# Optimization experiments

Measured on AMD Instinct MI355X. Metric: run time of the kernel, lower is better.

## Reference

```python
import jax, jax.numpy as jnp
import numpy as np

N_NODES = 50000
N_EDGES = 800000
F_DIM = 35   # num_features = in_channels = out_channels
K_HOPS = 3   # num_filters (diffusion order)


def _dconv(xcat, src, dst, w_fwd, w_bwd, theta, bias, n):
    """Dual-direction diffusion convolution: sum_k T_fwd^k X theta[0,k] + T_bwd^k X theta[1,k] + b.
    xcat: [n, Cin]; theta: [2, K, Cin, Cout]; w_fwd/w_bwd: [E] normalized edge weights."""
    out = xcat @ (theta[0, 0] + theta[1, 0]) + bias  # k=0 term (identity hop)
    xf = xcat
    xb = xcat
    for k in range(1, theta.shape[1]):
        # forward diffusion: aggregate src -> dst with out-degree normalization
        xf = jax.ops.segment_sum(w_fwd[:, None] * xf[src], dst, num_segments=n)
        # backward diffusion: aggregate dst -> src with in-degree normalization
        xb = jax.ops.segment_sum(w_bwd[:, None] * xb[dst], src, num_segments=n)
        out = out + xf @ theta[0, k] + xb @ theta[1, k]
    return out


def _cell(x, h, src, dst, wf, wb, tz, bz, tr, br, tc, bc, n):
    """DCRNN GRU cell with diffusion convolutions as the gate transforms."""
    xh = jnp.concatenate([x, h], axis=-1)  # [n, 2F]
    z = jax.nn.sigmoid(_dconv(xh, src, dst, wf, wb, tz, bz, n))
    r = jax.nn.sigmoid(_dconv(xh, src, dst, wf, wb, tr, br, n))
    c = jnp.tanh(_dconv(jnp.concatenate([x, r * h], axis=-1), src, dst, wf, wb, tc, bc, n))
    return z * h + (1.0 - z) * c


def setup_inputs() -> dict:
    key = jax.random.key(0)
    ks = jax.random.split(key, 12)
    x = jax.random.normal(ks[0], (N_NODES, F_DIM), dtype=jnp.float32)
    edge_index = jax.random.randint(ks[1], (2, N_EDGES), 0, N_NODES)
    edge_weight = jax.random.uniform(ks[2], (N_EDGES,), dtype=jnp.float32)
    cin = 2 * F_DIM
    s = 1.0 / np.sqrt(cin)
    u = lambda k, sh: jax.random.uniform(k, sh, jnp.float32, -s, s)
    theta_z = u(ks[3], (2, K_HOPS, cin, F_DIM)); b_z = u(ks[4], (F_DIM,))
    theta_r = u(ks[5], (2, K_HOPS, cin, F_DIM)); b_r = u(ks[6], (F_DIM,))
    theta_c = u(ks[7], (2, K_HOPS, cin, F_DIM)); b_c = u(ks[8], (F_DIM,))
    sl = 1.0 / np.sqrt(F_DIM)
    W_lin = jax.random.uniform(ks[9], (F_DIM, 1), jnp.float32, -sl, sl)
    b_lin = jax.random.uniform(ks[10], (1,), jnp.float32, -sl, sl)
    return dict(x=x, edge_index=edge_index, edge_weight=edge_weight,
                theta_z=theta_z, b_z=b_z, theta_r=theta_r, b_r=b_r,
                theta_c=theta_c, b_c=b_c, W_lin=W_lin, b_lin=b_lin)


def reference(x, edge_index, edge_weight, theta_z, b_z, theta_r, b_r, theta_c, b_c, W_lin, b_lin):
    n = x.shape[0]
    src, dst = edge_index[0], edge_index[1]
    # learned/normalized adjacency A (forward + backward transition weights)
    deg_out = jax.ops.segment_sum(edge_weight, src, num_segments=n)
    deg_in = jax.ops.segment_sum(edge_weight, dst, num_segments=n)
    wf = edge_weight / jnp.where(deg_out[src] > 0, deg_out[src], 1.0)
    wb = edge_weight / jnp.where(deg_in[dst] > 0, deg_in[dst], 1.0)
    A = jnp.stack([wf, wb])  # [2, E]
    h = jnp.zeros_like(x)
    # recurrent cell called twice (second call reuses hidden state and A)
    h = _cell(x, h, src, dst, wf, wb, theta_z, b_z, theta_r, b_r, theta_c, b_c, n)
    h = _cell(x, h, src, dst, wf, wb, theta_z, b_z, theta_r, b_r, theta_c, b_c, n)
    out = jax.nn.relu(h @ W_lin + b_lin)  # [n, 1]
    return out, A
```

## Files before the change

### kernel.cpp

```cpp
#include <hip/hip_runtime.h>
#include <hip/hip_fp16.h>

#define NF 35
#define HS 36
#define TMAT 2450
#define ZCOLS 384
#define ZUSED 360
#define CCOLS 192
#define CUSED 180


__global__ void degree2_k(const int* __restrict__ src, const int* __restrict__ dst,
                          unsigned int* __restrict__ cntF2, unsigned int* __restrict__ cntB2,
                          int* __restrict__ rankF, int* __restrict__ rankB, int E) {
    int e = blockIdx.x * blockDim.x + threadIdx.x;
    if (e < E) {
        int d = dst[e], s = src[e];
        int shd = (d & 1) * 16, shs = (s & 1) * 16;
        unsigned int o1 = atomicAdd(&cntF2[d >> 1], 1u << shd);
        rankF[e] = (int)((o1 >> shd) & 0xFFFFu);
        unsigned int o2 = atomicAdd(&cntB2[s >> 1], 1u << shs);
        rankB[e] = (int)((o2 >> shs) & 0xFFFFu);
    }
}

__global__ __launch_bounds__(1024) void scan2_k(const unsigned int* __restrict__ cntF2,
                                                const unsigned int* __restrict__ cntB2,
                                                int* __restrict__ rowF,
                                                int* __restrict__ rowB, int n) {
    const unsigned int* cnt = blockIdx.x ? cntB2 : cntF2;
    int* row = blockIdx.x ? rowB : rowF;
    __shared__ int wsum[16];
    __shared__ int carry_s;
    int lane = threadIdx.x & 63, wid = threadIdx.x >> 6;
    if (threadIdx.x == 0) carry_s = 0;
    __syncthreads();
    for (int base = 0; base < n; base += 1024) {
        int i = base + threadIdx.x;
        int v = 0;
        if (i < n) v = (int)((cnt[i >> 1] >> ((i & 1) * 16)) & 0xFFFFu);
        int s = v;
        for (int off = 1; off < 64; off <<= 1) {
            int t = __shfl_up(s, off, 64);
            if (lane >= off) s += t;
        }
        if (lane == 63) wsum[wid] = s;
        __syncthreads();
        if (wid == 0) {
            int t = (lane < 16) ? wsum[lane] : 0;
            int ss = t;
            for (int off = 1; off < 16; off <<= 1) {
                int u = __shfl_up(ss, off, 64);
                if (lane >= off) ss += u;
            }
            if (lane < 16) wsum[lane] = ss - t;
        }
        __syncthreads();
        if (i < n) row[i] = carry_s + wsum[wid] + s - v;
        __syncthreads();
        if (threadIdx.x == 1023) carry_s += wsum[15] + s;
        __syncthreads();
    }
    if (threadIdx.x == 0) row[n] = carry_s;
}

__global__ void scatter2_k(const int* __restrict__ src, const int* __restrict__ dst,
                           const float* __restrict__ w,
                           const int* __restrict__ rankF, const int* __restrict__ rankB,
                           const int* __restrict__ rowF, const int* __restrict__ rowB,
                           int2* __restrict__ pairF, int2* __restrict__ pairB, int E) {
    int e = blockIdx.x * blockDim.x + threadIdx.x;
    if (e < E) {
        int s = src[e], d = dst[e];
        int wb = __float_as_int(w[e]);
        pairF[rowF[d] + rankF[e]] = make_int2(s, wb);
        pairB[rowB[s] + rankB[e]] = make_int2(d, wb);
    }
}

__global__ void segdeg_k(const int* __restrict__ rowF, const int* __restrict__ rowB,
                         const int2* __restrict__ pairF, const int2* __restrict__ pairB,
                         float* __restrict__ deg_in, float* __restrict__ deg_out, int n) {
    int i = blockIdx.x * blockDim.x + threadIdx.x;
    if (i >= n) return;
    float a = 0.f;
    for (int p = rowF[i]; p < rowF[i + 1]; ++p) a += __int_as_float(pairF[p].y);
    deg_in[i] = a;
    float b = 0.f;
    for (int p = rowB[i]; p < rowB[i + 1]; ++p) b += __int_as_float(pairB[p].y);
    deg_out[i] = b;
}

__global__ void norm_k(const int* __restrict__ src, const int* __restrict__ dst,
                       const float* __restrict__ w, const float* __restrict__ deg_out,
                       const float* __restrict__ deg_in,
                       const int2* __restrict__ pairF, const int2* __restrict__ pairB,
                       unsigned int* __restrict__ pFp, unsigned int* __restrict__ pBp,
                       float* __restrict__ wf, float* __restrict__ wb, int E) {
    int e = blockIdx.x * blockDim.x + threadIdx.x;
    if (e >= E) return;
    float ww = w[e];
    float a = deg_out[src[e]];
    float b = deg_in[dst[e]];
    wf[e] = ww / (a > 0.f ? a : 1.f);
    wb[e] = ww / (b > 0.f ? b : 1.f);
    int2 pa = pairF[e];
    float da = deg_out[pa.x];
    float wa = __int_as_float(pa.y) / (da > 0.f ? da : 1.f);
    pFp[e] = (unsigned int)pa.x |
             ((unsigned int)__half_as_ushort(__float2half_rn(wa)) << 16);
    int2 pb = pairB[e];
    float db = deg_in[pb.x];
    float wbv = __int_as_float(pb.y) / (db > 0.f ? db : 1.f);
    pBp[e] = (unsigned int)pb.x |
             ((unsigned int)__half_as_ushort(__float2half_rn(wbv)) << 16);
}


__global__ void pack_k(const float* __restrict__ tz, const float* __restrict__ tr_,
                       const float* __restrict__ tc, const float* __restrict__ bz,
                       const float* __restrict__ br, const float* __restrict__ bc,
                       float* __restrict__ PZ, float* __restrict__ PC) {
    int i = blockIdx.x * 256 + threadIdx.x;
    const int tot1 = 71 * ZCOLS;
    if (i < tot1) {
        int r = i / ZCOLS, j = i - r * ZCOLS;
        int s = j / 36, jl = j - s * 36;
        float v = 0.f;
        if (s < 10 && jl < 35) {
            int zr = s & 1;
            const float* th = zr ? tr_ : tz;
            int grp = s >> 1;
            if (r < 70) {
                if (grp == 0) v = th[r * 35 + jl] + th[3 * TMAT + r * 35 + jl];
                else {
                    int off = (grp == 1) ? 1 : (grp == 2) ? 2 : (grp == 3) ? 4 : 5;
                    v = th[off * TMAT + r * 35 + jl];
                }
            } else if (grp == 0) {
                v = zr ? br[jl] : bz[jl];
            }
        }
        PZ[i] = v;
    } else {
        int i2 = i - tot1;
        if (i2 < 71 * CCOLS) {
            int r = i2 / CCOLS, j = i2 - r * CCOLS;
            int s = j / 36, jl = j - s * 36;
            float v = 0.f;
            if (s < 5 && jl < 35) {
                if (r < 70) {
                    if (s == 0) v = tc[r * 35 + jl] + tc[3 * TMAT + r * 35 + jl];
                    else {
                        int off = (s == 1) ? 1 : (s == 2) ? 2 : (s == 3) ? 4 : 5;
                        v = tc[off * TMAT + r * 35 + jl];
                    }
                } else if (s == 0) v = bc[jl];
            }
            PC[i2] = v;
        }
    }
}


__device__ __forceinline__ uint2 pack4h(float4 a) {
    __half2 lo = __floats2half2_rn(a.x, a.y);
    __half2 hi = __floats2half2_rn(a.z, a.w);
    uint2 r;
    r.x = *(unsigned int*)&lo;
    r.y = *(unsigned int*)&hi;
    return r;
}

__device__ __forceinline__ void fma4h(float* acc, uint2 v, float w) {
    const __half2* hp = (const __half2*)&v;
#pragma unroll
    for (int k = 0; k < 2; ++k) {
        float2 f = __half22float2(hp[k]);
        acc[2 * k] += w * f.x;
        acc[2 * k + 1] += w * f.y;
    }
}

__device__ __forceinline__ void ld12h(float* a, const char* p) {
    uint2 v0 = *(const uint2*)p, v1 = *(const uint2*)(p + 8), v2 = *(const uint2*)(p + 16);
    for (int k = 0; k < 12; ++k) a[k] = 0.f;
    fma4h(a, v0, 1.f); fma4h(a + 4, v1, 1.f); fma4h(a + 8, v2, 1.f);
}

__device__ __forceinline__ void st12h(const float* a, char* p) {
    *(uint2*)p = pack4h(make_float4(a[0], a[1], a[2], a[3]));
    *(uint2*)(p + 8) = pack4h(make_float4(a[4], a[5], a[6], a[7]));
    *(uint2*)(p + 16) = pack4h(make_float4(a[8], a[9], a[10], a[11]));
}

__device__ __forceinline__ float hw(unsigned int e) {
    return __half2float(__ushort_as_half((unsigned short)(e >> 16)));
}

__device__ __forceinline__ void gath(float* acc, const char* slab, int off,
                                     const int* __restrict__ rp,
                                     const unsigned int* __restrict__ pp, int row) {
    int p = rp[row], p1 = rp[row + 1];
    for (; p + 3 < p1; p += 4) {
        unsigned int e0 = pp[p], e1 = pp[p + 1], e2 = pp[p + 2], e3 = pp[p + 3];
        const char* s0 = slab + (size_t)(e0 & 0xFFFFu) * 72 + off;
        const char* s1 = slab + (size_t)(e1 & 0xFFFFu) * 72 + off;
        const char* s2 = slab + (size_t)(e2 & 0xFFFFu) * 72 + off;
        const char* s3 = slab + (size_t)(e3 & 0xFFFFu) * 72 + off;
        uint2 a0 = *(const uint2*)s0, a1 = *(const uint2*)(s0 + 8), a2 = *(const uint2*)(s0 + 16);
        uint2 b0 = *(const uint2*)s1, b1 = *(const uint2*)(s1 + 8), b2 = *(const uint2*)(s1 + 16);
        uint2 c0 = *(const uint2*)s2, c1 = *(const uint2*)(s2 + 8), c2 = *(const uint2*)(s2 + 16);
        uint2 d0 = *(const uint2*)s3, d1 = *(const uint2*)(s3 + 8), d2 = *(const uint2*)(s3 + 16);
        float w0 = hw(e0), w1 = hw(e1), w2 = hw(e2), w3 = hw(e3);
        fma4h(acc, a0, w0); fma4h(acc + 4, a1, w0); fma4h(acc + 8, a2, w0);
        fma4h(acc, b0, w1); fma4h(acc + 4, b1, w1); fma4h(acc + 8, b2, w1);
        fma4h(acc, c0, w2); fma4h(acc + 4, c1, w2); fma4h(acc + 8, c2, w2);
        fma4h(acc, d0, w3); fma4h(acc + 4, d1, w3); fma4h(acc + 8, d2, w3);
    }
    for (; p < p1; ++p) {
        unsigned int e0 = pp[p];
        const char* s0 = slab + (size_t)(e0 & 0xFFFFu) * 72 + off;
        float w0 = hw(e0);
        fma4h(acc, *(const uint2*)s0, w0);
        fma4h(acc + 4, *(const uint2*)(s0 + 8), w0);
        fma4h(acc + 8, *(const uint2*)(s0 + 16), w0);
    }
}


template <int WCOLS, int USED>
__device__ __forceinline__ void gemm_store(const float* sxr, const float* __restrict__ W,
                                           char* OUT, size_t slb, int grow, bool valid,
                                           int wid) {
#pragma unroll
    for (int jt = 0; jt < WCOLS / 64; ++jt) {
        int j0 = __builtin_amdgcn_readfirstlane(jt * 64 + wid * 16);
        if (j0 >= USED) continue;
        const float4* bw = (const float4*)(W + (size_t)70 * WCOLS + j0);
        float4 a0 = bw[0], a1 = bw[1], a2 = bw[2], a3 = bw[3];
        for (int c = 0; c < 70; ++c) {
            float v = sxr[c];
            const float4* wr = (const float4*)(W + (size_t)c * WCOLS + j0);
            float4 w0 = wr[0], w1 = wr[1], w2 = wr[2], w3 = wr[3];
            a0.x += v * w0.x; a0.y += v * w0.y; a0.z += v * w0.z; a0.w += v * w0.w;
            a1.x += v * w1.x; a1.y += v * w1.y; a1.z += v * w1.z; a1.w += v * w1.w;
            a2.x += v * w2.x; a2.y += v * w2.y; a2.z += v * w2.z; a2.w += v * w2.w;
            a3.x += v * w3.x; a3.y += v * w3.y; a3.z += v * w3.z; a3.w += v * w3.w;
        }
        if (valid) {
            float4 as[4] = {a0, a1, a2, a3};
#pragma unroll
            for (int g = 0; g < 4; ++g) {
                int jc = j0 + 4 * g;
                if (jc >= USED) break;
                int s = jc / 36, off = jc - s * 36;
                *(uint2*)(OUT + (size_t)s * slb + (size_t)grow * 72 + off * 2) =
                    pack4h(as[g]);
            }
        }
    }
}


__global__ __launch_bounds__(256) void mm_z_k(const float* __restrict__ x,
                                              const float* __restrict__ h,
                                              const float* __restrict__ W,
                                              char* __restrict__ zS, int n) {
    __shared__ float sx[64 * 73];
    int row0 = blockIdx.x * 64;
    for (int t = threadIdx.x; t < 64 * 35; t += 256) {
        int rl = t / 35, c = t - rl * 35;
        int grow = row0 + rl;
        sx[rl * 73 + c] = (grow < n) ? x[(size_t)grow * 35 + c] : 0.f;
    }
    for (int t = threadIdx.x; t < 64 * 35; t += 256) {
        int rl = t / 35, c = t - rl * 35;
        int grow = row0 + rl;
        sx[rl * 73 + 35 + c] = (grow < n) ? h[(size_t)grow * HS + c] : 0.f;
    }
    __syncthreads();
    int lane = threadIdx.x & 63;
    int wid = threadIdx.x >> 6;
    int grow = row0 + lane;
    gemm_store<ZCOLS, ZUSED>(&sx[lane * 73], W, zS, (size_t)n * 72, grow, grow < n, wid);
}


__global__ __launch_bounds__(256) void hopAz_k(char* __restrict__ zS,
                                               const int* __restrict__ rowF,
                                               const int* __restrict__ rowB,
                                               const unsigned int* __restrict__ pF,
                                               const unsigned int* __restrict__ pB,
                                               int n) {
    size_t slb = (size_t)n * 72;
    int i = blockIdx.x * 256 + threadIdx.x;
    int row = i / 3, t = i - row * 3;
    int off = 24 * t;
    bool act = (i < n * 3);
    float acc[12];
#define HOPA_PHASE(DSTS, SRCS, RP, PP)                           \
    if (act) {                                                   \
        char* wp = zS + (DSTS)*slb + (size_t)row * 72 + off;     \
        ld12h(acc, wp);                                          \
        gath(acc, zS + (SRCS)*slb, off, RP, PP, row);            \
        st12h(acc, wp);                                          \
    }                                                            \
    __syncthreads();
    HOPA_PHASE(2, 4, rowF, pF)
    HOPA_PHASE(3, 5, rowF, pF)
    HOPA_PHASE(6, 8, rowB, pB)
    HOPA_PHASE(7, 9, rowB, pB)
#undef HOPA_PHASE
}


__global__ __launch_bounds__(256) void hopBz_k(char* __restrict__ zS,
                                               const int* __restrict__ rowF,
                                               const int* __restrict__ rowB,
                                               const unsigned int* __restrict__ pF,
                                               const unsigned int* __restrict__ pB,
                                               int n) {
    size_t slb = (size_t)n * 72;
    int i = blockIdx.x * 256 + threadIdx.x;
    int row = i / 3, t = i - row * 3;
    int off = 24 * t;
    bool act = (i < n * 3);
    float acc[12];
    if (act) {
        ld12h(acc, zS + (size_t)row * 72 + off);
        gath(acc, zS + 2 * slb, off, rowF, pF, row);
    }
    __syncthreads();
    if (act) {
        gath(acc, zS + 6 * slb, off, rowB, pB, row);
#pragma unroll
        for (int k = 0; k < 12; ++k) acc[k] = 1.f / (1.f + expf(-acc[k]));
        st12h(acc, zS + (size_t)row * 72 + off);
    }
    __syncthreads();
    if (act) {
        ld12h(acc, zS + slb + (size_t)row * 72 + off);
        gath(acc, zS + 3 * slb, off, rowF, pF, row);
    }
    __syncthreads();
    if (act) {
        gath(acc, zS + 7 * slb, off, rowB, pB, row);
#pragma unroll
        for (int k = 0; k < 12; ++k) acc[k] = 1.f / (1.f + expf(-acc[k]));
        st12h(acc, zS + slb + (size_t)row * 72 + off);
    }
}


__global__ __launch_bounds__(256) void mmc_k(const float* __restrict__ x,
                                             const float* __restrict__ h,
                                             const char* __restrict__ zS,
                                             const float* __restrict__ W,
                                             char* __restrict__ cS, int n) {
    __shared__ float sx[64 * 73];
    size_t slb = (size_t)n * 72;
    int row0 = blockIdx.x * 64;
    for (int t = threadIdx.x; t < 64 * 35; t += 256) {
        int rl = t / 35, c = t - rl * 35;
        int grow = row0 + rl;
        sx[rl * 73 + c] = (grow < n) ? x[(size_t)grow * 35 + c] : 0.f;
    }
    for (int t = threadIdx.x; t < 64 * 35; t += 256) {
        int rl = t / 35, c = t - rl * 35;
        int grow = row0 + rl;
        float v = 0.f;
        if (grow < n) {
            float r = __half2float(*(const __half*)(zS + slb + (size_t)grow * 72 + 2 * c));
            v = r * h[(size_t)grow * HS + c];
        }
        sx[rl * 73 + 35 + c] = v;
    }
    __syncthreads();
    int lane = threadIdx.x & 63;
    int wid = threadIdx.x >> 6;
    int grow = row0 + lane;
    gemm_store<CCOLS, CUSED>(&sx[lane * 73], W, cS, slb, grow, grow < n, wid);
}


__global__ __launch_bounds__(256) void hopAc_k(char* __restrict__ cS,
                                               const int* __restrict__ rowF,
                                               const int* __restrict__ rowB,
                                               const unsigned int* __restrict__ pF,
                                               const unsigned int* __restrict__ pB,
                                               int n) {
    size_t slb = (size_t)n * 72;
    int i = blockIdx.x * 256 + threadIdx.x;
    int row = i / 3, t = i - row * 3;
    int off = 24 * t;
    bool act = (i < n * 3);
    float acc[12];
    if (act) {
        char* wp = cS + slb + (size_t)row * 72 + off;
        ld12h(acc, wp);
        gath(acc, cS + 2 * slb, off, rowF, pF, row);
        st12h(acc, wp);
    }
    __syncthreads();
    if (act) {
        char* wp = cS + 3 * slb + (size_t)row * 72 + off;
        ld12h(acc, wp);
        gath(acc, cS + 4 * slb, off, rowB, pB, row);
        st12h(acc, wp);
    }
}


template <int FIN>
__global__ __launch_bounds__(256) void fch_k(const float* __restrict__ x,
                                             float* __restrict__ h,
                                             const char* __restrict__ cS,
                                             const char* __restrict__ zS,
                                             const float* __restrict__ W,
                                             char* __restrict__ zOut,
                                             const int* __restrict__ rowF,
                                             const int* __restrict__ rowB,
                                             const unsigned int* __restrict__ pF,
                                             const unsigned int* __restrict__ pB,
                                             const float* __restrict__ Wl,
                                             const float* __restrict__ bl,
                                             float* __restrict__ out, int n) {
    __shared__ float sx[64 * 73];
    __shared__ float sred[64 * 3];
    size_t slb = (size_t)n * 72;
    int row0 = blockIdx.x * 64;
    int u = threadIdx.x;
    int rl = u / 3, t = u - rl * 3;
    int row = row0 + rl;
    int off = 24 * t;
    bool act = (u < 192 && row < n);
    float acc[12];
    if (act) {
        ld12h(acc, cS + (size_t)row * 72 + off);
        gath(acc, cS + slb, off, rowF, pF, row);
    }
    __syncthreads();
    if (act) {
        gath(acc, cS + 3 * slb, off, rowB, pB, row);
        float zv[12];
        ld12h(zv, zS + (size_t)row * 72 + off);
        float* hp = h + (size_t)row * HS + 12 * t;
        float4 h0 = *(float4*)hp, h1 = *(float4*)(hp + 4), h2 = *(float4*)(hp + 8);
        float hv[12] = {h0.x, h0.y, h0.z, h0.w, h1.x, h1.y, h1.z, h1.w,
                        h2.x, h2.y, h2.z, h2.w};
#pragma unroll
        for (int k = 0; k < 12; ++k) {
            float c = tanhf(acc[k]);
            hv[k] = zv[k] * hv[k] + (1.f - zv[k]) * c;
        }
        if (FIN == 0) {
            *(float4*)hp = make_float4(hv[0], hv[1], hv[2], hv[3]);
            *(float4*)(hp + 4) = make_float4(hv[4], hv[5], hv[6], hv[7]);
            *(float4*)(hp + 8) = make_float4(hv[8], hv[9], hv[10], hv[11]);
#pragma unroll
            for (int k = 0; k < 12; ++k) sx[rl * 73 + 35 + 12 * t + k] = hv[k];
        } else {
            float part = 0.f;
#pragma unroll
            for (int k = 0; k < 12; ++k) {
                int col = 12 * t + k;
                if (col < 35) part += hv[k] * Wl[col];
            }
            sred[rl * 3 + t] = part;
        }
    }
    __syncthreads();
    if (FIN == 1) {
        if (u < 64) {
            int r2 = row0 + u;
            if (r2 < n) {
                float s = bl[0] + sred[u * 3] + sred[u * 3 + 1] + sred[u * 3 + 2];
                out[r2] = fmaxf(s, 0.f);
            }
        }
        return;
    }
    for (int t2 = threadIdx.x; t2 < 64 * 35; t2 += 256) {
        int rl2 = t2 / 35, c = t2 - rl2 * 35;
        int grow = row0 + rl2;
        sx[rl2 * 73 + c] = (grow < n) ? x[(size_t)grow * 35 + c] : 0.f;
    }
    __syncthreads();
    int lane = threadIdx.x & 63;
    int wid = threadIdx.x >> 6;
    int grow = row0 + lane;
    gemm_store<ZCOLS, ZUSED>(&sx[lane * 73], W, zOut, slb, grow, grow < n, wid);
}


extern "C" void kernel_launch(void* const* d_in, const int* in_sizes, int n_in,
                              void* d_out, int out_size, void* d_ws, size_t ws_size,
                              hipStream_t stream) {
    const float* x   = (const float*)d_in[0];
    const int*   ei  = (const int*)d_in[1];
    const float* w   = (const float*)d_in[2];
    const float* tz  = (const float*)d_in[3];
    const float* bz  = (const float*)d_in[4];
    const float* tr_ = (const float*)d_in[5];
    const float* br  = (const float*)d_in[6];
    const float* tc  = (const float*)d_in[7];
    const float* bc  = (const float*)d_in[8];
    const float* Wl  = (const float*)d_in[9];
    const float* bl  = (const float*)d_in[10];

    const int n = in_sizes[0] / NF;
    const int E = in_sizes[2];
    const int* src = ei;
    const int* dst = ei + E;

    float* out = (float*)d_out;
    float* wf = out + n;
    float* wb = wf + E;

    char* p = (char*)d_ws;
    auto alloc = [&](size_t bytes) {
        char* r = p;
        p += (bytes + 15) & ~(size_t)15;
        return r;
    };
    int2* pairF = (int2*)alloc((size_t)E * 8);
    int2* pairB = (int2*)alloc((size_t)E * 8);
    unsigned int* pFp = (unsigned int*)alloc((size_t)E * 4);
    unsigned int* pBp = (unsigned int*)alloc((size_t)E * 4);
    int* rowF = (int*)alloc((size_t)(n + 1) * 4);
    int* rowB = (int*)alloc((size_t)(n + 1) * 4);
    unsigned int* cntF2 = (unsigned int*)alloc((size_t)((n + 1) / 2 + 4) * 4);
    unsigned int* cntB2 = (unsigned int*)alloc((size_t)((n + 1) / 2 + 4) * 4);
    float* deg_in  = (float*)alloc((size_t)n * 4);
    float* deg_out = (float*)alloc((size_t)n * 4);
    float* h  = (float*)alloc((size_t)n * HS * 4);
    char* zS  = alloc((size_t)n * 72 * 10);
    char* cS  = alloc((size_t)n * 72 * 5);
    float* PZ = (float*)alloc((size_t)71 * ZCOLS * 4);
    float* PC = (float*)alloc((size_t)71 * CCOLS * 4);
    int* rankF = (int*)zS;
    int* rankB = rankF + E;

    const int gridE = (E + 255) / 256;
    const int gridN = (n + 255) / 256;
    const int g64 = (n + 63) / 64;
    const int g3 = (n * 3 + 255) / 256;
    const size_t cntBytes = ((size_t)((n + 1) / 2 + 4) * 4 + 15) & ~(size_t)15;

    hipMemsetAsync(cntF2, 0, 2 * cntBytes, stream);
    hipMemsetAsync(h, 0, (size_t)n * HS * sizeof(float), stream);
    degree2_k<<<gridE, 256, 0, stream>>>(src, dst, cntF2, cntB2, rankF, rankB, E);
    scan2_k<<<2, 1024, 0, stream>>>(cntF2, cntB2, rowF, rowB, n);
    scatter2_k<<<gridE, 256, 0, stream>>>(src, dst, w, rankF, rankB, rowF, rowB,
                                          pairF, pairB, E);
    segdeg_k<<<gridN, 256, 0, stream>>>(rowF, rowB, pairF, pairB, deg_in, deg_out, n);
    norm_k<<<gridE, 256, 0, stream>>>(src, dst, w, deg_out, deg_in, pairF, pairB,
                                      pFp, pBp, wf, wb, E);
    pack_k<<<(71 * (ZCOLS + CCOLS) + 255) / 256, 256, 0, stream>>>(tz, tr_, tc,
                                                                   bz, br, bc, PZ, PC);

    mm_z_k<<<g64, 256, 0, stream>>>(x, h, PZ, zS, n);
    hopAz_k<<<g3, 256, 0, stream>>>(zS, rowF, rowB, pFp, pBp, n);
    hopBz_k<<<g3, 256, 0, stream>>>(zS, rowF, rowB, pFp, pBp, n);
    mmc_k<<<g64, 256, 0, stream>>>(x, h, zS, PC, cS, n);
    hopAc_k<<<g3, 256, 0, stream>>>(cS, rowF, rowB, pFp, pBp, n);
    fch_k<0><<<g64, 256, 0, stream>>>(x, h, cS, zS, PZ, zS, rowF, rowB, pFp, pBp,
                                      Wl, bl, out, n);
    hopAz_k<<<g3, 256, 0, stream>>>(zS, rowF, rowB, pFp, pBp, n);
    hopBz_k<<<g3, 256, 0, stream>>>(zS, rowF, rowB, pFp, pBp, n);
    mmc_k<<<g64, 256, 0, stream>>>(x, h, zS, PC, cS, n);
    hopAc_k<<<g3, 256, 0, stream>>>(cS, rowF, rowB, pFp, pBp, n);
    fch_k<1><<<g64, 256, 0, stream>>>(x, h, cS, zS, PZ, zS, rowF, rowB, pFp, pBp,
                                      Wl, bl, out, n);
}
```

Measured before the change: 752.9 us.

## Split hop gathers into 8-byte-per-thread passes, unfuse gate kernel, skip zero hidden

The hop kernels now give each thread an 8-byte chunk (9 threads per row instead of 3) and spread independent diffusion passes across blockIdx.y instead of running them serially with __syncthreads, which raises parallelism and memory-level concurrency in the gather. The fused final-gate plus next-z GEMM kernel is replaced by a separate gate/update kernel, a templated z GEMM that skips the h half when h is zero, and a small output kernel. In exchange there are more index loads per row, smaller gathers per thread, and extra launches and round trips through global memory.

```diff
diff --git a/kernel.cpp b/kernel.cpp
--- a/kernel.cpp
+++ b/kernel.cpp
@@ -172,59 +172,50 @@
     return r;
 }
 
-__device__ __forceinline__ void fma4h(float* acc, uint2 v, float w) {
-    const __half2* hp = (const __half2*)&v;
-#pragma unroll
-    for (int k = 0; k < 2; ++k) {
-        float2 f = __half22float2(hp[k]);
-        acc[2 * k] += w * f.x;
-        acc[2 * k + 1] += w * f.y;
-    }
-}
-
-__device__ __forceinline__ void ld12h(float* a, const char* p) {
-    uint2 v0 = *(const uint2*)p, v1 = *(const uint2*)(p + 8), v2 = *(const uint2*)(p + 16);
-    for (int k = 0; k < 12; ++k) a[k] = 0.f;
-    fma4h(a, v0, 1.f); fma4h(a + 4, v1, 1.f); fma4h(a + 8, v2, 1.f);
-}
-
-__device__ __forceinline__ void st12h(const float* a, char* p) {
+__device__ __forceinline__ void fma2h(float* a, unsigned int v, float w) {
+    float2 f = __half22float2(*(__half2*)&v);
+    a[0] += w * f.x;
+    a[1] += w * f.y;
+}
+
+__device__ __forceinline__ void fma4u2(float* a, uint2 v, float w) {
+    fma2h(a, v.x, w);
+    fma2h(a + 2, v.y, w);
+}
+
+__device__ __forceinline__ void ld4h(float* a, const char* p) {
+    uint2 v = *(const uint2*)p;
+    a[0] = 0.f; a[1] = 0.f; a[2] = 0.f; a[3] = 0.f;
+    fma4u2(a, v, 1.f);
+}
+
+__device__ __forceinline__ void st4h(const float* a, char* p) {
     *(uint2*)p = pack4h(make_float4(a[0], a[1], a[2], a[3]));
-    *(uint2*)(p + 8) = pack4h(make_float4(a[4], a[5], a[6], a[7]));
-    *(uint2*)(p + 16) = pack4h(make_float4(a[8], a[9], a[10], a[11]));
 }
 
 __device__ __forceinline__ float hw(unsigned int e) {
     return __half2float(__ushort_as_half((unsigned short)(e >> 16)));
 }
 
-__device__ __forceinline__ void gath(float* acc, const char* slab, int off,
-                                     const int* __restrict__ rp,
-                                     const unsigned int* __restrict__ pp, int row) {
+__device__ __forceinline__ void gath8(float* acc, const char* slab, int off,
+                                      const int* __restrict__ rp,
+                                      const unsigned int* __restrict__ pp, int row) {
     int p = rp[row], p1 = rp[row + 1];
     for (; p + 3 < p1; p += 4) {
         unsigned int e0 = pp[p], e1 = pp[p + 1], e2 = pp[p + 2], e3 = pp[p + 3];
-        const char* s0 = slab + (size_t)(e0 & 0xFFFFu) * 72 + off;
-        const char* s1 = slab + (size_t)(e1 & 0xFFFFu) * 72 + off;
-        const char* s2 = slab + (size_t)(e2 & 0xFFFFu) * 72 + off;
-        const char* s3 = slab + (size_t)(e3 & 0xFFFFu) * 72 + off;
-        uint2 a0 = *(const uint2*)s0, a1 = *(const uint2*)(s0 + 8), a2 = *(const uint2*)(s0 + 16);
-        uint2 b0 = *(const uint2*)s1, b1 = *(const uint2*)(s1 + 8), b2 = *(const uint2*)(s1 + 16);
-        uint2 c0 = *(const uint2*)s2, c1 = *(const uint2*)(s2 + 8), c2 = *(const uint2*)(s2 + 16);
-        uint2 d0 = *(const uint2*)s3, d1 = *(const uint2*)(s3 + 8), d2 = *(const uint2*)(s3 + 16);
-        float w0 = hw(e0), w1 = hw(e1), w2 = hw(e2), w3 = hw(e3);
-        fma4h(acc, a0, w0); fma4h(acc + 4, a1, w0); fma4h(acc + 8, a2, w0);
-        fma4h(acc, b0, w1); fma4h(acc + 4, b1, w1); fma4h(acc + 8, b2, w1);
-        fma4h(acc, c0, w2); fma4h(acc + 4, c1, w2); fma4h(acc + 8, c2, w2);
-        fma4h(acc, d0, w3); fma4h(acc + 4, d1, w3); fma4h(acc + 8, d2, w3);
+        uint2 v0 = *(const uint2*)(slab + (size_t)(e0 & 0xFFFFu) * 72 + off);
+        uint2 v1 = *(const uint2*)(slab + (size_t)(e1 & 0xFFFFu) * 72 + off);
+        uint2 v2 = *(const uint2*)(slab + (size_t)(e2 & 0xFFFFu) * 72 + off);
+        uint2 v3 = *(const uint2*)(slab + (size_t)(e3 & 0xFFFFu) * 72 + off);
+        fma4u2(acc, v0, hw(e0));
+        fma4u2(acc, v1, hw(e1));
+        fma4u2(acc, v2, hw(e2));
+        fma4u2(acc, v3, hw(e3));
     }
     for (; p < p1; ++p) {
         unsigned int e0 = pp[p];
-        const char* s0 = slab + (size_t)(e0 & 0xFFFFu) * 72 + off;
-        float w0 = hw(e0);
-        fma4h(acc, *(const uint2*)s0, w0);
-        fma4h(acc + 4, *(const uint2*)(s0 + 8), w0);
-        fma4h(acc + 8, *(const uint2*)(s0 + 16), w0);
+        uint2 v0 = *(const uint2*)(slab + (size_t)(e0 & 0xFFFFu) * 72 + off);
+        fma4u2(acc, v0, hw(e0));
     }
 }
 
@@ -232,14 +223,14 @@
 template <int WCOLS, int USED>
 __device__ __forceinline__ void gemm_store(const float* sxr, const float* __restrict__ W,
                                            char* OUT, size_t slb, int grow, bool valid,
-                                           int wid) {
+                                           int wid, int kdim) {
 #pragma unroll
     for (int jt = 0; jt < WCOLS / 64; ++jt) {
         int j0 = __builtin_amdgcn_readfirstlane(jt * 64 + wid * 16);
         if (j0 >= USED) continue;
         const float4* bw = (const float4*)(W + (size_t)70 * WCOLS + j0);
         float4 a0 = bw[0], a1 = bw[1], a2 = bw[2], a3 = bw[3];
-        for (int c = 0; c < 70; ++c) {
+        for (int c = 0; c < kdim; ++c) {
             float v = sxr[c];
             const float4* wr = (const float4*)(W + (size_t)c * WCOLS + j0);
             float4 w0 = wr[0], w1 = wr[1], w2 = wr[2], w3 = wr[3];
@@ -263,6 +254,7 @@
 }
 
 
+template <int H0>
 __global__ __launch_bounds__(256) void mm_z_k(const float* __restrict__ x,
                                               const float* __restrict__ h,
                                               const float* __restrict__ W,
@@ -274,82 +266,19 @@
         int grow = row0 + rl;
         sx[rl * 73 + c] = (grow < n) ? x[(size_t)grow * 35 + c] : 0.f;
     }
-    for (int t = threadIdx.x; t < 64 * 35; t += 256) {
-        int rl = t / 35, c = t - rl * 35;
-        int grow = row0 + rl;
-        sx[rl * 73 + 35 + c] = (grow < n) ? h[(size_t)grow * HS + c] : 0.f;
+    if (!H0) {
+        for (int t = threadIdx.x; t < 64 * 35; t += 256) {
+            int rl = t / 35, c = t - rl * 35;
+            int grow = row0 + rl;
+            sx[rl * 73 + 35 + c] = (grow < n) ? h[(size_t)grow * HS + c] : 0.f;
+        }
     }
     __syncthreads();
     int lane = threadIdx.x & 63;
     int wid = threadIdx.x >> 6;
     int grow = row0 + lane;
-    gemm_store<ZCOLS, ZUSED>(&sx[lane * 73], W, zS, (size_t)n * 72, grow, grow < n, wid);
-}
-
-
-__global__ __launch_bounds__(256) void hopAz_k(char* __restrict__ zS,
-                                               const int* __restrict__ rowF,
-                                               const int* __restrict__ rowB,
-                                               const unsigned int* __restrict__ pF,
-                                               const unsigned int* __restrict__ pB,
-                                               int n) {
-    size_t slb = (size_t)n * 72;
-    int i = blockIdx.x * 256 + threadIdx.x;
-    int row = i / 3, t = i - row * 3;
-    int off = 24 * t;
-    bool act = (i < n * 3);
-    float acc[12];
-#define HOPA_PHASE(DSTS, SRCS, RP, PP)                           \
-    if (act) {                                                   \
-        char* wp = zS + (DSTS)*slb + (size_t)row * 72 + off;     \
-        ld12h(acc, wp);                                          \
-        gath(acc, zS + (SRCS)*slb, off, RP, PP, row);            \
-        st12h(acc, wp);                                          \
-    }                                                            \
-    __syncthreads();
-    HOPA_PHASE(2, 4, rowF, pF)
-    HOPA_PHASE(3, 5, rowF, pF)
-    HOPA_PHASE(6, 8, rowB, pB)
-    HOPA_PHASE(7, 9, rowB, pB)
-#undef HOPA_PHASE
-}
-
-
-__global__ __launch_bounds__(256) void hopBz_k(char* __restrict__ zS,
-                                               const int* __restrict__ rowF,
-                                               const int* __restrict__ rowB,
-                                               const unsigned int* __restrict__ pF,
-                                               const unsigned int* __restrict__ pB,
-                                               int n) {
-    size_t slb = (size_t)n * 72;
-    int i = blockIdx.x * 256 + threadIdx.x;
-    int row = i / 3, t = i - row * 3;
-    int off = 24 * t;
-    bool act = (i < n * 3);
-    float acc[12];
-    if (act) {
-        ld12h(acc, zS + (size_t)row * 72 + off);
-        gath(acc, zS + 2 * slb, off, rowF, pF, row);
-    }
-    __syncthreads();
-    if (act) {
-        gath(acc, zS + 6 * slb, off, rowB, pB, row);
-#pragma unroll
-        for (int k = 0; k < 12; ++k) acc[k] = 1.f / (1.f + expf(-acc[k]));
-        st12h(acc, zS + (size_t)row * 72 + off);
-    }
-    __syncthreads();
-    if (act) {
-        ld12h(acc, zS + slb + (size_t)row * 72 + off);
-        gath(acc, zS + 3 * slb, off, rowF, pF, row);
-    }
-    __syncthreads();
-    if (act) {
-        gath(acc, zS + 7 * slb, off, rowB, pB, row);
-#pragma unroll
-        for (int k = 0; k < 12; ++k) acc[k] = 1.f / (1.f + expf(-acc[k]));
-        st12h(acc, zS + slb + (size_t)row * 72 + off);
-    }
+    gemm_store<ZCOLS, ZUSED>(&sx[lane * 73], W, zS, (size_t)n * 72, grow, grow < n,
+                             wid, H0 ? 35 : 70);
 }
 
 
@@ -380,9 +309,54 @@
     int lane = threadIdx.x & 63;
     int wid = threadIdx.x >> 6;
     int grow = row0 + lane;
-    gemm_store<CCOLS, CUSED>(&sx[lane * 73], W, cS, slb, grow, grow < n, wid);
-}
-
+    gemm_store<CCOLS, CUSED>(&sx[lane * 73], W, cS, slb, grow, grow < n, wid, 70);
+}
+
+
+__global__ __launch_bounds__(256) void hopAz_k(char* __restrict__ zS,
+                                               const int* __restrict__ rowF,
+                                               const int* __restrict__ rowB,
+                                               const unsigned int* __restrict__ pF,
+                                               const unsigned int* __restrict__ pB,
+                                               int n) {
+    int i = blockIdx.x * 256 + threadIdx.x;
+    if (i >= n * 9) return;
+    size_t slb = (size_t)n * 72;
+    int pass = blockIdx.y;
+    const int* rp = (pass < 2) ? rowF : rowB;
+    const unsigned int* pp = (pass < 2) ? pF : pB;
+    int dstS = (pass == 0) ? 2 : (pass == 1) ? 3 : (pass == 2) ? 6 : 7;
+    int srcS = dstS + 2;
+    int row = i / 9, t = i - row * 9;
+    int off = 8 * t;
+    char* wp = zS + (size_t)dstS * slb + (size_t)row * 72 + off;
+    float acc[4];
+    ld4h(acc, wp);
+    gath8(acc, zS + (size_t)srcS * slb, off, rp, pp, row);
+    st4h(acc, wp);
+}
+
+__global__ __launch_bounds__(256) void hopBz_k(char* __restrict__ zS,
+                                               const int* __restrict__ rowF,
+                                               const int* __restrict__ rowB,
+                                               const unsigned int* __restrict__ pF,
+                                               const unsigned int* __restrict__ pB,
+                                               int n) {
+    int i = blockIdx.x * 256 + threadIdx.x;
+    if (i >= n * 9) return;
+    size_t slb = (size_t)n * 72;
+    int g = blockIdx.y;
+    int row = i / 9, t = i - row * 9;
+    int off = 8 * t;
+    char* wp = zS + (size_t)g * slb + (size_t)row * 72 + off;
+    float acc[4];
+    ld4h(acc, wp);
+    gath8(acc, zS + (size_t)(2 + g) * slb, off, rowF, pF, row);
+    gath8(acc, zS + (size_t)(6 + g) * slb, off, rowB, pB, row);
+#pragma unroll
+    for (int k = 0; k < 4; ++k) acc[k] = 1.f / (1.f + expf(-acc[k]));
+    st4h(acc, wp);
+}
 
 __global__ __launch_bounds__(256) void hopAc_k(char* __restrict__ cS,
                                                const int* __restrict__ rowF,
@@ -390,107 +364,63 @@
                                                const unsigned int* __restrict__ pF,
                                                const unsigned int* __restrict__ pB,
                                                int n) {
+    int i = blockIdx.x * 256 + threadIdx.x;
+    if (i >= n * 9) return;
     size_t slb = (size_t)n * 72;
+    int pass = blockIdx.y;
+    const int* rp = pass ? rowB : rowF;
+    const unsigned int* pp = pass ? pB : pF;
+    int dstS = pass ? 3 : 1;
+    int srcS = pass ? 4 : 2;
+    int row = i / 9, t = i - row * 9;
+    int off = 8 * t;
+    char* wp = cS + (size_t)dstS * slb + (size_t)row * 72 + off;
+    float acc[4];
+    ld4h(acc, wp);
+    gath8(acc, cS + (size_t)srcS * slb, off, rp, pp, row);
+    st4h(acc, wp);
+}
+
+__global__ __launch_bounds__(256) void hopBcg_k(const char* __restrict__ cS,
+                                                const char* __restrict__ zS,
+                                                const int* __restrict__ rowF,
+                                                const int* __restrict__ rowB,
+                                                const unsigned int* __restrict__ pF,
+                                                const unsigned int* __restrict__ pB,
+                                                float* __restrict__ h, int n) {
     int i = blockIdx.x * 256 + threadIdx.x;
-    int row = i / 3, t = i - row * 3;
-    int off = 24 * t;
-    bool act = (i < n * 3);
-    float acc[12];
-    if (act) {
-        char* wp = cS + slb + (size_t)row * 72 + off;
-        ld12h(acc, wp);
-        gath(acc, cS + 2 * slb, off, rowF, pF, row);
-        st12h(acc, wp);
-    }
-    __syncthreads();
-    if (act) {
-        char* wp = cS + 3 * slb + (size_t)row * 72 + off;
-        ld12h(acc, wp);
-        gath(acc, cS + 4 * slb, off, rowB, pB, row);
-        st12h(acc, wp);
-    }
-}
-
-
-template <int FIN>
-__global__ __launch_bounds__(256) void fch_k(const float* __restrict__ x,
-                                             float* __restrict__ h,
-                                             const char* __restrict__ cS,
-                                             const char* __restrict__ zS,
-                                             const float* __restrict__ W,
-                                             char* __restrict__ zOut,
-                                             const int* __restrict__ rowF,
-                                             const int* __restrict__ rowB,
-                                             const unsigned int* __restrict__ pF,
-                                             const unsigned int* __restrict__ pB,
-                                             const float* __restrict__ Wl,
-                                             const float* __restrict__ bl,
-                                             float* __restrict__ out, int n) {
-    __shared__ float sx[64 * 73];
-    __shared__ float sred[64 * 3];
+    if (i >= n * 9) return;
     size_t slb = (size_t)n * 72;
-    int row0 = blockIdx.x * 64;
-    int u = threadIdx.x;
-    int rl = u / 3, t = u - rl * 3;
-    int row = row0 + rl;
-    int off = 24 * t;
-    bool act = (u < 192 && row < n);
-    float acc[12];
-    if (act) {
-        ld12h(acc, cS + (size_t)row * 72 + off);
-        gath(acc, cS + slb, off, rowF, pF, row);
-    }
-    __syncthreads();
-    if (act) {
-        gath(acc, cS + 3 * slb, off, rowB, pB, row);
-        float zv[12];
-        ld12h(zv, zS + (size_t)row * 72 + off);
-        float* hp = h + (size_t)row * HS + 12 * t;
-        float4 h0 = *(float4*)hp, h1 = *(float4*)(hp + 4), h2 = *(float4*)(hp + 8);
-        float hv[12] = {h0.x, h0.y, h0.z, h0.w, h1.x, h1.y, h1.z, h1.w,
-                        h2.x, h2.y, h2.z, h2.w};
+    int row = i / 9, t = i - row * 9;
+    int off = 8 * t;
+    float acc[4];
+    ld4h(acc, cS + (size_t)row * 72 + off);
+    gath8(acc, cS + slb, off, rowF, pF, row);
+    gath8(acc, cS + 3 * slb, off, rowB, pB, row);
+    float zv[4];
+    ld4h(zv, zS + (size_t)row * 72 + off);
+    float* hp = h + (size_t)row * HS + 4 * t;
+    float4 h4 = *(float4*)hp;
+    float hv[4] = {h4.x, h4.y, h4.z, h4.w};
 #pragma unroll
-        for (int k = 0; k < 12; ++k) {
-            float c = tanhf(acc[k]);
-            hv[k] = zv[k] * hv[k] + (1.f - zv[k]) * c;
-        }
-        if (FIN == 0) {
-            *(float4*)hp = make_float4(hv[0], hv[1], hv[2], hv[3]);
-            *(float4*)(hp + 4) = make_float4(hv[4], hv[5], hv[6], hv[7]);
-            *(float4*)(hp + 8) = make_float4(hv[8], hv[9], hv[10], hv[11]);
+    for (int k = 0; k < 4; ++k) {
+        float c = tanhf(acc[k]);
+        hv[k] = zv[k] * hv[k] + (1.f - zv[k]) * c;
+    }
+    *(float4*)hp = make_float4(hv[0], hv[1], hv[2], hv[3]);
+}
+
+
+__global__ void final_k(const float* __restrict__ h, const float* __restrict__ Wl,
+                        const float* __restrict__ bl, float* __restrict__ out, int n) {
+    int i = blockIdx.x * blockDim.x + threadIdx.x;
+    if (i < n) {
+        float s = bl[0];
+        const float* hr = h + (size_t)i * HS;
 #pragma unroll
-            for (int k = 0; k < 12; ++k) sx[rl * 73 + 35 + 12 * t + k] = hv[k];
-        } else {
-            float part = 0.f;
-#pragma unroll
-            for (int k = 0; k < 12; ++k) {
-                int col = 12 * t + k;
-                if (col < 35) part += hv[k] * Wl[col];
-            }
-            sred[rl * 3 + t] = part;
-        }
-    }
-    __syncthreads();
-    if (FIN == 1) {
-        if (u < 64) {
-            int r2 = row0 + u;
-            if (r2 < n) {
-                float s = bl[0] + sred[u * 3] + sred[u * 3 + 1] + sred[u * 3 + 2];
-                out[r2] = fmaxf(s, 0.f);
-            }
-        }
-        return;
-    }
-    for (int t2 = threadIdx.x; t2 < 64 * 35; t2 += 256) {
-        int rl2 = t2 / 35, c = t2 - rl2 * 35;
-        int grow = row0 + rl2;
-        sx[rl2 * 73 + c] = (grow < n) ? x[(size_t)grow * 35 + c] : 0.f;
-    }
-    __syncthreads();
-    int lane = threadIdx.x & 63;
-    int wid = threadIdx.x >> 6;
-    int grow = row0 + lane;
-    gemm_store<ZCOLS, ZUSED>(&sx[lane * 73], W, zOut, slb, grow, grow < n, wid);
+        for (int j = 0; j < NF; j++) s += hr[j] * Wl[j];
+        out[i] = fmaxf(s, 0.f);
+    }
 }
 
 
@@ -545,7 +475,7 @@
     const int gridE = (E + 255) / 256;
     const int gridN = (n + 255) / 256;
     const int g64 = (n + 63) / 64;
-    const int g3 = (n * 3 + 255) / 256;
+    const int g9 = (n * 9 + 255) / 256;
     const size_t cntBytes = ((size_t)((n + 1) / 2 + 4) * 4 + 15) & ~(size_t)15;
 
     hipMemsetAsync(cntF2, 0, 2 * cntBytes, stream);
@@ -560,17 +490,18 @@
     pack_k<<<(71 * (ZCOLS + CCOLS) + 255) / 256, 256, 0, stream>>>(tz, tr_, tc,
                                                                    bz, br, bc, PZ, PC);
 
-    mm_z_k<<<g64, 256, 0, stream>>>(x, h, PZ, zS, n);
-    hopAz_k<<<g3, 256, 0, stream>>>(zS, rowF, rowB, pFp, pBp, n);
-    hopBz_k<<<g3, 256, 0, stream>>>(zS, rowF, rowB, pFp, pBp, n);
+    mm_z_k<1><<<g64, 256, 0, stream>>>(x, h, PZ, zS, n);
+    hopAz_k<<<dim3(g9, 4), 256, 0, stream>>>(zS, rowF, rowB, pFp, pBp, n);
+    hopBz_k<<<dim3(g9, 2), 256, 0, stream>>>(zS, rowF, rowB, pFp, pBp, n);
     mmc_k<<<g64, 256, 0, stream>>>(x, h, zS, PC, cS, n);
-    hopAc_k<<<g3, 256, 0, stream>>>(cS, rowF, rowB, pFp, pBp, n);
-    fch_k<0><<<g64, 256, 0, stream>>>(x, h, cS, zS, PZ, zS, rowF, rowB, pFp, pBp,
-                                      Wl, bl, out, n);
-    hopAz_k<<<g3, 256, 0, stream>>>(zS, rowF, rowB, pFp, pBp, n);
-    hopBz_k<<<g3, 256, 0, stream>>>(zS, rowF, rowB, pFp, pBp, n);
+    hopAc_k<<<dim3(g9, 2), 256, 0, stream>>>(cS, rowF, rowB, pFp, pBp, n);
+    hopBcg_k<<<g9, 256, 0, stream>>>(cS, zS, rowF, rowB, pFp, pBp, h, n);
+    mm_z_k<0><<<g64, 256, 0, stream>>>(x, h, PZ, zS, n);
+    hopAz_k<<<dim3(g9, 4), 256, 0, stream>>>(zS, rowF, rowB, pFp, pBp, n);
+    hopBz_k<<<dim3(g9, 2), 256, 0, stream>>>(zS, rowF, rowB, pFp, pBp, n);
     mmc_k<<<g64, 256, 0, stream>>>(x, h, zS, PC, cS, n);
-    hopAc_k<<<g3, 256, 0, stream>>>(cS, rowF, rowB, pFp, pBp, n);
-    fch_k<1><<<g64, 256, 0, stream>>>(x, h, cS, zS, PZ, zS, rowF, rowB, pFp, pBp,
-                                      Wl, bl, out, n);
-}
+    hopAc_k<<<dim3(g9, 2), 256, 0, stream>>>(cS, rowF, rowB, pFp, pBp, n);
+    hopBcg_k<<<g9, 256, 0, stream>>>(cS, zS, rowF, rowB, pFp, pBp, h, n);
+
+    final_k<<<gridN, 256, 0, stream>>>(h, Wl, bl, out, n);
+}
```

Measured after the change: 676.2 us. 1.11x faster.
